# Performance work log

Hardware: AMD Instinct MI355X
Metric: run time of the kernel (lower is better)

## Reference

```python
import jax, jax.numpy as jnp
import numpy as np

N = 25000      # nodes
E = 400000     # edges
IN = 1024      # in_channels
FC = 128       # feature_channels
ADD = 20       # additional_channels
MID = (FC + ADD) // 4   # 37, fc1 output (heads=4)
OUT = 3
EPS = 1e-5
NEG_SLOPE = 0.01


def setup_inputs() -> dict:
    key = jax.random.key(0)
    ks = jax.random.split(key, 16)
    d = {}
    d["features"] = jax.random.normal(ks[0], (N, IN), dtype=jnp.float32)
    d["edges"] = jax.random.randint(ks[1], (2, E), 0, N, dtype=jnp.int64)
    d["edges2"] = jax.random.randint(ks[2], (2, 1000), 0, N, dtype=jnp.int64)
    d["edge_features"] = jax.random.normal(ks[3], (E, 1), dtype=jnp.float32)
    d["additional_feature"] = jax.random.normal(ks[4], (N, ADD), dtype=jnp.float32)
    # SAGEConv params: lin_l (neighbor path, with bias), lin_r (root path, no bias)
    s = 1.0 / np.sqrt(IN)
    d["Wl"] = jax.random.uniform(ks[5], (FC, IN), jnp.float32, -s, s)
    d["bl"] = jax.random.uniform(ks[6], (FC,), jnp.float32, -s, s)
    d["Wr"] = jax.random.uniform(ks[7], (FC, IN), jnp.float32, -s, s)
    s1 = 1.0 / np.sqrt(FC + ADD)
    d["W1"] = jax.random.uniform(ks[8], (MID, FC + ADD), jnp.float32, -s1, s1)
    d["b1"] = jax.random.uniform(ks[9], (MID,), jnp.float32, -s1, s1)
    s2 = 1.0 / np.sqrt(MID)
    d["W2"] = jax.random.uniform(ks[10], (OUT, MID), jnp.float32, -s2, s2)
    d["b2"] = jax.random.uniform(ks[11], (OUT,), jnp.float32, -s2, s2)
    # BatchNorm1d (eval mode -> running stats)
    d["gamma"] = jnp.ones((MID,), jnp.float32)
    d["beta"] = jnp.zeros((MID,), jnp.float32)
    d["run_mean"] = jax.random.normal(ks[12], (MID,), dtype=jnp.float32) * 0.1
    d["run_var"] = jnp.abs(jax.random.normal(ks[13], (MID,), dtype=jnp.float32)) * 0.1 + 1.0
    return d


def reference(features, edges, edges2, edge_features, additional_feature,
              Wl, bl, Wr, W1, b1, W2, b2, gamma, beta, run_mean, run_var):
    src, dst = edges[0], edges[1]  # PyG: messages flow source -> target
    # scatter-mean of neighbor features onto targets
    agg = jax.ops.segment_sum(features[src], dst, num_segments=N)        # [N, IN]
    deg = jax.ops.segment_sum(jnp.ones((E,), features.dtype), dst, num_segments=N)
    agg = agg / jnp.maximum(deg, 1.0)[:, None]
    # SAGEConv: lin_l(mean_neigh) + lin_r(x)
    x = agg @ Wl.T + bl + features @ Wr.T                                 # [N, FC]
    x = jnp.where(x >= 0, x, NEG_SLOPE * x)                               # leaky_relu
    # dropout is identity in eval mode
    x = jnp.concatenate([x, additional_feature], axis=1) @ W1.T + b1      # [N, MID]
    x = jnp.maximum(x, 0.0)                                               # relu
    x = gamma * (x - run_mean) * jax.lax.rsqrt(run_var + EPS) + beta      # BN eval
    return x @ W2.T + b2                                                  # [N, OUT]
```

## Files before the change

### kernel.cpp

```cpp
#include <hip/hip_runtime.h>

#define N_NODES 25000
#define N_EDGES 400000
#define IN_CH 1024
#define FC 128
#define ADD_CH 20
#define XCH 148
#define MID 37
#define OUT_CH 3
#define MAXDEG 64

typedef short bf16x8 __attribute__((ext_vector_type(8)));
typedef float f32x4 __attribute__((ext_vector_type(4)));

__device__ __forceinline__ unsigned int f2bf(float x) {
    unsigned int u = __builtin_bit_cast(unsigned int, x);
    unsigned int lsb = (u >> 16) & 1u;
    u += 0x7fffu + lsb;
    return u >> 16;
}
__device__ __forceinline__ unsigned int pkbf(float a, float b) {
    return f2bf(a) | (f2bf(b) << 16);
}
__device__ __forceinline__ float bflo(unsigned int v) {
    return __builtin_bit_cast(float, v << 16);
}
__device__ __forceinline__ float bfhi(unsigned int v) {
    return __builtin_bit_cast(float, v & 0xffff0000u);
}

#define WSWZ_B 16
#define BUILD_B 1563

__global__ __launch_bounds__(256) void prep_kernel(const float* __restrict__ Wl,
                                                   const float* __restrict__ Wr,
                                                   const int* __restrict__ edges,
                                                   ushort* __restrict__ Wpk,
                                                   int* __restrict__ cursor,
                                                   int* __restrict__ col) {
    int b = blockIdx.x, t = threadIdx.x;
    if (b < WSWZ_B) {
        int w = t >> 6, lane = t & 63, l15 = lane & 15, q8 = (lane >> 4) * 8;
        int ch = b * 16 + l15;
        const float* src = (ch < FC) ? (Wl + (size_t)ch * IN_CH)
                                     : (Wr + (size_t)(ch - FC) * IN_CH);
        #pragma unroll
        for (int j = 0; j < 8; ++j) {
            int kt = w * 8 + j;
            float4 lo = *(const float4*)(src + kt * 32 + q8);
            float4 hi = *(const float4*)(src + kt * 32 + q8 + 4);
            uint4 pk;
            pk.x = pkbf(lo.x, lo.y); pk.y = pkbf(lo.z, lo.w);
            pk.z = pkbf(hi.x, hi.y); pk.w = pkbf(hi.z, hi.w);
            ((uint4*)Wpk)[(size_t)(b * 32 + kt) * 64 + lane] = pk;
        }
    } else {
        int e = (b - WSWZ_B) * 256 + t;
        if (e < N_EDGES) {
            int dst = edges[N_EDGES + e];
            int pos = atomicAdd(&cursor[dst], 1);
            if (pos < MAXDEG) col[dst * MAXDEG + pos] = edges[e];
        }
    }
}

__global__ __launch_bounds__(256) void gemm_kernel(const float* __restrict__ A,
                                                   const ushort* __restrict__ Wpk,
                                                   ushort* __restrict__ Py,
                                                   ushort* __restrict__ Pz) {
    __shared__ __align__(16) ushort Fs[2 * 32 * 64 * 8];
    int t = threadIdx.x, w = t >> 6, lane = t & 63;
    int l15 = lane & 15, q = lane >> 4;
    int m0 = blockIdx.x * 32;

    const bf16x8* Wf = (const bf16x8*)Wpk + (size_t)(w * 4) * 32 * 64 + lane;
    bf16x8 aw[4], an[4];
    #pragma unroll
    for (int cf = 0; cf < 4; ++cf) aw[cf] = Wf[(size_t)cf * 32 * 64];

    {
        int r = t >> 3;
        int p0 = t & 7;
        int row = m0 + r; if (row >= N_NODES) row = N_NODES - 1;
        const float* src = A + (size_t)row * IN_CH;
        int g = r >> 4, l = r & 15;
        #pragma unroll
        for (int m = 0; m < 16; ++m) {
            int o = m * 8 + p0;
            int kt = o >> 2, qq = o & 3;
            float4 lo = *(const float4*)(src + o * 8);
            float4 hi = *(const float4*)(src + o * 8 + 4);
            uint4 pk;
            pk.x = pkbf(lo.x, lo.y); pk.y = pkbf(lo.z, lo.w);
            pk.z = pkbf(hi.x, hi.y); pk.w = pkbf(hi.z, hi.w);
            *(uint4*)&Fs[(size_t)((g * 32 + kt) * 64 + qq * 16 + l) * 8] = pk;
        }
    }
    __syncthreads();

    const bf16x8* Ff = (const bf16x8*)Fs + lane;
    f32x4 acc[4][2] = {};
    for (int kt = 0; kt < 32; ++kt) {
        if (kt + 1 < 32) {
            #pragma unroll
            for (int cf = 0; cf < 4; ++cf) an[cf] = Wf[(size_t)(cf * 32 + kt + 1) * 64];
        }
        bf16x8 b0 = Ff[(size_t)(0 * 32 + kt) * 64];
        bf16x8 b1 = Ff[(size_t)(1 * 32 + kt) * 64];
        #pragma unroll
        for (int cf = 0; cf < 4; ++cf) {
            acc[cf][0] = __builtin_amdgcn_mfma_f32_16x16x32_bf16(aw[cf], b0, acc[cf][0], 0, 0, 0);
            acc[cf][1] = __builtin_amdgcn_mfma_f32_16x16x32_bf16(aw[cf], b1, acc[cf][1], 0, 0, 0);
        }
        #pragma unroll
        for (int cf = 0; cf < 4; ++cf) aw[cf] = an[cf];
    }
    #pragma unroll
    for (int g = 0; g < 2; ++g) {
        int node = m0 + g * 16 + l15;
        if (node < N_NODES) {
            ushort* base = (w < 2) ? (Py + (size_t)node * FC + w * 64)
                                   : (Pz + (size_t)node * FC + (w - 2) * 64);
            #pragma unroll
            for (int cf = 0; cf < 4; ++cf) {
                f32x4 v = acc[cf][g];
                uint2 pk;
                pk.x = pkbf(v[0], v[1]);
                pk.y = pkbf(v[2], v[3]);
                *(uint2*)(base + cf * 16 + q * 4) = pk;
            }
        }
    }
}

__global__ __launch_bounds__(256) void fused_tail(const ushort* __restrict__ Py,
                                                  const ushort* __restrict__ Pz,
                                                  const int* __restrict__ deg,
                                                  const int* __restrict__ col,
                                                  const float* __restrict__ addf,
                                                  const float* __restrict__ bl,
                                                  const float* __restrict__ W1,
                                                  const float* __restrict__ b1,
                                                  const float* __restrict__ W2,
                                                  const float* __restrict__ b2,
                                                  const float* __restrict__ gamma,
                                                  const float* __restrict__ beta,
                                                  const float* __restrict__ rmean,
                                                  const float* __restrict__ rvar,
                                                  float* __restrict__ out) {
    __shared__ float W1s[XCH][MID + 3];
    __shared__ float xbuf[4][XCH + 4];
    __shared__ float hbuf[4][MID + 3];
    int t = threadIdx.x;
    for (int idx = t; idx < MID * XCH; idx += 256) {
        int j = idx / XCH, k = idx - j * XCH;
        W1s[k][j] = W1[idx];
    }
    __syncthreads();
    int w = t >> 6, lane = t & 63;
    int n = blockIdx.x * 4 + w;
    bool valid = (n < N_NODES);
    int d = valid ? deg[n] : 0;
    if (d > MAXDEG) d = MAXDEG;
    int g = lane >> 4, c16 = lane & 15;
    float s[8] = {0.f, 0.f, 0.f, 0.f, 0.f, 0.f, 0.f, 0.f};
    if (d > 0) {
        int cidx = col[n * MAXDEG + (lane < d ? lane : 0)];
        for (int i = 0; i < d; i += 16) {
            int e[4];
            uint4 v[4];
            #pragma unroll
            for (int j = 0; j < 4; ++j) {
                int ee = i + g + j * 4;
                e[j] = __shfl(cidx, (ee < d) ? ee : 0);
            }
            #pragma unroll
            for (int j = 0; j < 4; ++j)
                v[j] = *(const uint4*)&Py[(size_t)e[j] * FC + c16 * 8];
            #pragma unroll
            for (int j = 0; j < 4; ++j) {
                if (i + g + j * 4 < d) {
                    s[0] += bflo(v[j].x); s[1] += bfhi(v[j].x);
                    s[2] += bflo(v[j].y); s[3] += bfhi(v[j].y);
                    s[4] += bflo(v[j].z); s[5] += bfhi(v[j].z);
                    s[6] += bflo(v[j].w); s[7] += bfhi(v[j].w);
                }
            }
        }
        #pragma unroll
        for (int r = 0; r < 8; ++r) {
            s[r] += __shfl_xor(s[r], 16);
            s[r] += __shfl_xor(s[r], 32);
        }
    }
    if (valid) {
        if (lane < 16) {
            #pragma unroll
            for (int r = 0; r < 8; ++r) xbuf[w][lane * 8 + r] = s[r];
        }
        float invd = 1.0f / (float)(d > 1 ? d : 1);
        unsigned int vr = *(const unsigned int*)&Pz[(size_t)n * FC + lane * 2];
        float x0 = xbuf[w][2 * lane] * invd + bl[2 * lane] + bflo(vr);
        float x1 = xbuf[w][2 * lane + 1] * invd + bl[2 * lane + 1] + bfhi(vr);
        x0 = (x0 >= 0.f) ? x0 : 0.01f * x0;
        x1 = (x1 >= 0.f) ? x1 : 0.01f * x1;
        xbuf[w][2 * lane] = x0;
        xbuf[w][2 * lane + 1] = x1;
        if (lane < ADD_CH) xbuf[w][FC + lane] = addf[(size_t)n * ADD_CH + lane];
        if (lane < MID) {
            float h = b1[lane];
            #pragma unroll 4
            for (int k = 0; k < XCH; ++k) h += W1s[k][lane] * xbuf[w][k];
            h = fmaxf(h, 0.0f);
            h = gamma[lane] * (h - rmean[lane]) * rsqrtf(rvar[lane] + 1e-5f) + beta[lane];
            hbuf[w][lane] = h;
        }
        if (lane < OUT_CH) {
            float o = b2[lane];
            #pragma unroll
            for (int j = 0; j < MID; ++j) o += W2[lane * MID + j] * hbuf[w][j];
            out[(size_t)n * OUT_CH + lane] = o;
        }
    }
}


extern "C" void kernel_launch(void* const* d_in, const int* in_sizes, int n_in,
                              void* d_out, int out_size, void* d_ws, size_t ws_size,
                              hipStream_t stream) {
    const float* features = (const float*)d_in[0];
    const int*   edges    = (const int*)d_in[1];
    const float* addf     = (const float*)d_in[4];
    const float* Wl       = (const float*)d_in[5];
    const float* bl       = (const float*)d_in[6];
    const float* Wr       = (const float*)d_in[7];
    const float* W1       = (const float*)d_in[8];
    const float* b1       = (const float*)d_in[9];
    const float* W2       = (const float*)d_in[10];
    const float* b2       = (const float*)d_in[11];
    const float* gamma    = (const float*)d_in[12];
    const float* beta     = (const float*)d_in[13];
    const float* rmean    = (const float*)d_in[14];
    const float* rvar     = (const float*)d_in[15];
    float* out = (float*)d_out;

    char* ws = (char*)d_ws;
    size_t off = 0;
    ushort* Py = (ushort*)(ws + off);     off += (size_t)N_NODES * FC * 2;
    ushort* Pz = (ushort*)(ws + off);     off += (size_t)N_NODES * FC * 2;
    ushort* Wpk = (ushort*)(ws + off);    off += (size_t)16 * 32 * 64 * 16;
    int* cursor = (int*)(ws + off);       off += (size_t)N_NODES * 4;
    int* col = (int*)(ws + off);          off += (size_t)N_NODES * MAXDEG * 4;

    (void)hipMemsetAsync(cursor, 0, (size_t)N_NODES * 4, stream);

    prep_kernel<<<WSWZ_B + BUILD_B, 256, 0, stream>>>(Wl, Wr, edges, Wpk, cursor, col);

    gemm_kernel<<<(N_NODES + 31) / 32, 256, 0, stream>>>(features, Wpk, Py, Pz);

    fused_tail<<<(N_NODES + 3) / 4, 256, 0, stream>>>(Py, Pz, cursor, col, addf, bl,
                                                      W1, b1, W2, b2, gamma, beta,
                                                      rmean, rvar, out);
}
```

Before: 299.1 us.

## Deepen GEMM prefetch, batch global loads, and swizzle LDS tile layout

The feature-to-LDS staging loop now issues all eight float4 pairs per half before converting and storing, which raises memory-level parallelism. The LDS layout is XOR-like rotated by quadrant to avoid bank conflicts on the store pattern. The main MFMA loop now prefetches two k-steps of weights and LDS fragments ahead instead of one. Launch bounds request two blocks per CU. The trade-off is higher register pressure, which may spill or cap occupancy.

```diff
diff --git a/kernel.cpp b/kernel.cpp
--- a/kernel.cpp
+++ b/kernel.cpp
@@ -64,19 +64,16 @@
     }
 }
 
-__global__ __launch_bounds__(256) void gemm_kernel(const float* __restrict__ A,
-                                                   const ushort* __restrict__ Wpk,
-                                                   ushort* __restrict__ Py,
-                                                   ushort* __restrict__ Pz) {
+__global__ __launch_bounds__(256, 2) void gemm_kernel(const float* __restrict__ A,
+                                                      const ushort* __restrict__ Wpk,
+                                                      ushort* __restrict__ Py,
+                                                      ushort* __restrict__ Pz) {
     __shared__ __align__(16) ushort Fs[2 * 32 * 64 * 8];
     int t = threadIdx.x, w = t >> 6, lane = t & 63;
     int l15 = lane & 15, q = lane >> 4;
     int m0 = blockIdx.x * 32;
 
     const bf16x8* Wf = (const bf16x8*)Wpk + (size_t)(w * 4) * 32 * 64 + lane;
-    bf16x8 aw[4], an[4];
-    #pragma unroll
-    for (int cf = 0; cf < 4; ++cf) aw[cf] = Wf[(size_t)cf * 32 * 64];
 
     {
         int r = t >> 3;
@@ -85,35 +82,66 @@
         const float* src = A + (size_t)row * IN_CH;
         int g = r >> 4, l = r & 15;
         #pragma unroll
-        for (int m = 0; m < 16; ++m) {
-            int o = m * 8 + p0;
-            int kt = o >> 2, qq = o & 3;
-            float4 lo = *(const float4*)(src + o * 8);
-            float4 hi = *(const float4*)(src + o * 8 + 4);
-            uint4 pk;
-            pk.x = pkbf(lo.x, lo.y); pk.y = pkbf(lo.z, lo.w);
-            pk.z = pkbf(hi.x, hi.y); pk.w = pkbf(hi.z, hi.w);
-            *(uint4*)&Fs[(size_t)((g * 32 + kt) * 64 + qq * 16 + l) * 8] = pk;
+        for (int h = 0; h < 2; ++h) {
+            float4 lo[8], hi[8];
+            #pragma unroll
+            for (int m = 0; m < 8; ++m) {
+                int o = (h * 8 + m) * 8 + p0;
+                lo[m] = *(const float4*)(src + o * 8);
+                hi[m] = *(const float4*)(src + o * 8 + 4);
+            }
+            #pragma unroll
+            for (int m = 0; m < 8; ++m) {
+                int o = (h * 8 + m) * 8 + p0;
+                int kt = o >> 2, qq = o & 3;
+                uint4 pk;
+                pk.x = pkbf(lo[m].x, lo[m].y); pk.y = pkbf(lo[m].z, lo[m].w);
+                pk.z = pkbf(hi[m].x, hi[m].y); pk.w = pkbf(hi[m].z, hi[m].w);
+                int u = (g * 32 + kt) * 64 + qq * 16 + ((l + qq) & 15);
+                *(uint4*)&Fs[(size_t)u * 8] = pk;
+            }
         }
     }
     __syncthreads();
 
-    const bf16x8* Ff = (const bf16x8*)Fs + lane;
+    int ru = q * 16 + ((l15 + q) & 15);
+    const bf16x8* F0 = (const bf16x8*)Fs + (0 * 32) * 64 + ru;
+    const bf16x8* F1 = (const bf16x8*)Fs + (1 * 32) * 64 + ru;
+
     f32x4 acc[4][2] = {};
-    for (int kt = 0; kt < 32; ++kt) {
-        if (kt + 1 < 32) {
-            #pragma unroll
-            for (int cf = 0; cf < 4; ++cf) an[cf] = Wf[(size_t)(cf * 32 + kt + 1) * 64];
-        }
-        bf16x8 b0 = Ff[(size_t)(0 * 32 + kt) * 64];
-        bf16x8 b1 = Ff[(size_t)(1 * 32 + kt) * 64];
-        #pragma unroll
-        for (int cf = 0; cf < 4; ++cf) {
-            acc[cf][0] = __builtin_amdgcn_mfma_f32_16x16x32_bf16(aw[cf], b0, acc[cf][0], 0, 0, 0);
-            acc[cf][1] = __builtin_amdgcn_mfma_f32_16x16x32_bf16(aw[cf], b1, acc[cf][1], 0, 0, 0);
-        }
-        #pragma unroll
-        for (int cf = 0; cf < 4; ++cf) aw[cf] = an[cf];
+    bf16x8 aw[2][4], an[2][4], bw[2][2], bn[2][2];
+    #pragma unroll
+    for (int cf = 0; cf < 4; ++cf) {
+        aw[0][cf] = Wf[(size_t)(cf * 32 + 0) * 64];
+        aw[1][cf] = Wf[(size_t)(cf * 32 + 1) * 64];
+    }
+    bw[0][0] = F0[0 * 64]; bw[0][1] = F1[0 * 64];
+    bw[1][0] = F0[1 * 64]; bw[1][1] = F1[1 * 64];
+
+    for (int kt = 0; kt < 32; kt += 2) {
+        int kn = kt + 2;
+        if (kn < 32) {
+            #pragma unroll
+            for (int cf = 0; cf < 4; ++cf) {
+                an[0][cf] = Wf[(size_t)(cf * 32 + kn) * 64];
+                an[1][cf] = Wf[(size_t)(cf * 32 + kn + 1) * 64];
+            }
+            bn[0][0] = F0[(size_t)kn * 64];       bn[0][1] = F1[(size_t)kn * 64];
+            bn[1][0] = F0[(size_t)(kn + 1) * 64]; bn[1][1] = F1[(size_t)(kn + 1) * 64];
+        }
+        #pragma unroll
+        for (int j = 0; j < 2; ++j)
+            #pragma unroll
+            for (int cf = 0; cf < 4; ++cf) {
+                acc[cf][0] = __builtin_amdgcn_mfma_f32_16x16x32_bf16(aw[j][cf], bw[j][0], acc[cf][0], 0, 0, 0);
+                acc[cf][1] = __builtin_amdgcn_mfma_f32_16x16x32_bf16(aw[j][cf], bw[j][1], acc[cf][1], 0, 0, 0);
+            }
+        #pragma unroll
+        for (int j = 0; j < 2; ++j) {
+            #pragma unroll
+            for (int cf = 0; cf < 4; ++cf) aw[j][cf] = an[j][cf];
+            bw[j][0] = bn[j][0]; bw[j][1] = bn[j][1];
+        }
     }
     #pragma unroll
     for (int g = 0; g < 2; ++g) {
```

New measurement: 295.1 us. Within noise of the previous version (-1.4%).
